# Kernel tuning notes

Measured on AMD Instinct MI355X. Metric: run time of the kernel, lower is better.

Reference implementation:

```python
import jax, jax.numpy as jnp
import numpy as np

N_NODES = 100000
N_EDGES = 1600000
N_GRAPHS = 512
F_IN = 20
HID = 128
OUT = HID // 2


def _glorot(key, shape):
    fan_in, fan_out = shape[0], shape[1]
    lim = float(np.sqrt(6.0 / (fan_in + fan_out)))
    return jax.random.uniform(key, shape, jnp.float32, -lim, lim)


def setup_inputs() -> dict:
    key = jax.random.key(0)
    ks = jax.random.split(key, 12)
    x = jax.random.normal(ks[0], (N_NODES, F_IN), jnp.float32)
    edge_index = jax.random.randint(ks[1], (2, N_EDGES), 0, N_NODES, dtype=jnp.int64)
    batch = jnp.sort(jax.random.randint(ks[2], (N_NODES,), 0, N_GRAPHS, dtype=jnp.int64))
    return {
        "x": x,
        "edge_index": edge_index,
        "batch": batch,
        "W1": _glorot(ks[3], (F_IN, HID)), "b1": jnp.zeros((HID,), jnp.float32),
        "W2": _glorot(ks[4], (HID, HID)), "b2": jnp.zeros((HID,), jnp.float32),
        "W3": _glorot(ks[5], (HID, HID)), "b3": jnp.zeros((HID,), jnp.float32),
        "Wout": _glorot(ks[6], (HID, OUT)), "bout": jnp.zeros((OUT,), jnp.float32),
    }


def _gcn_conv(x, W, b, src, dst, num_nodes):
    # PyG GCNConv: x' = D^{-1/2} (A + I) D^{-1/2} X W + b (self-loops already in src/dst)
    xw = x @ W                                                  # [N, H]
    ones = jnp.ones(src.shape[0], dtype=xw.dtype)
    deg = jax.ops.segment_sum(ones, dst, num_segments=num_nodes)
    dinv = jnp.where(deg > 0, jax.lax.rsqrt(deg), 0.0)          # [N]
    norm = dinv[src] * dinv[dst]                                # [E+N]
    msg = xw[src] * norm[:, None]                               # gather + scale
    return jax.ops.segment_sum(msg, dst, num_segments=num_nodes) + b


def reference(x, edge_index, batch, W1, b1, W2, b2, W3, b3, Wout, bout):
    num_nodes = x.shape[0]
    loops = jnp.arange(num_nodes, dtype=edge_index.dtype)
    src = jnp.concatenate([edge_index[0], loops])
    dst = jnp.concatenate([edge_index[1], loops])

    h = jax.nn.relu(_gcn_conv(x, W1, b1, src, dst, num_nodes))
    h = jax.nn.relu(_gcn_conv(h, W2, b2, src, dst, num_nodes))
    h = jax.nn.relu(_gcn_conv(h, W3, b3, src, dst, num_nodes))

    # global_mean_pool over graph ids
    sums = jax.ops.segment_sum(h, batch, num_segments=N_GRAPHS)
    counts = jax.ops.segment_sum(jnp.ones(num_nodes, h.dtype), batch, num_segments=N_GRAPHS)
    pooled = sums / jnp.maximum(counts, 1.0)[:, None]           # [G, H]
    return pooled @ Wout + bout                                 # [G, H//2]
```

## Files before the change

### kernel.cpp

```cpp
#include <hip/hip_runtime.h>
#include <hip/hip_fp16.h>

#define N_NODES 100000
#define N_EDGES 1600000
#define N_GRAPHS 512
#define F_IN 20
#define HID 128
#define OUT_F 64

#define BUCKETS 512
#define SPAN 196
#define BCAP 3500
#define EPB 4096

typedef _Float16 half8_t __attribute__((ext_vector_type(8)));
typedef float f32x4_t __attribute__((ext_vector_type(4)));
typedef unsigned int uv4 __attribute__((ext_vector_type(4)));

__device__ inline float4 h4_to_f4(uint2 u) {
    __half2 h0 = *(__half2*)&u.x;
    __half2 h1 = *(__half2*)&u.y;
    float2 f0 = __half22float2(h0);
    float2 f1 = __half22float2(h1);
    return make_float4(f0.x, f0.y, f1.x, f1.y);
}

__device__ inline float4 f4_from(unsigned a, unsigned b) {
    __half2 h0 = *(__half2*)&a;
    __half2 h1 = *(__half2*)&b;
    float2 f0 = __half22float2(h0);
    float2 f1 = __half22float2(h1);
    return make_float4(f0.x, f0.y, f1.x, f1.y);
}

__device__ inline void acc8(float4& aL, float4& aH, uv4 v) {
    float4 l_ = f4_from(v[0], v[1]);
    float4 h_ = f4_from(v[2], v[3]);
    aL.x += l_.x; aL.y += l_.y; aL.z += l_.z; aL.w += l_.w;
    aH.x += h_.x; aH.y += h_.y; aH.z += h_.z; aH.w += h_.w;
}

__global__ __launch_bounds__(512) void partition(const int* __restrict__ src,
                                                 const int* __restrict__ dst,
                                                 int* __restrict__ bpairs,
                                                 int* cur512) {
    __shared__ int lcnt[8][BUCKETS];
    __shared__ int woff[8][BUCKETS];
    int t = threadIdx.x;
    int wv = t >> 6;
    for (int i = t; i < 8 * BUCKETS; i += 512) ((int*)lcnt)[i] = 0;
    __syncthreads();
    int base = blockIdx.x * EPB;
    int myb[8], myp[8], myr[8];
#pragma unroll
    for (int i = 0; i < 8; ++i) {
        int e = base + i * 512 + t;
        int b = -1, p = 0, rk = 0;
        if (e < N_EDGES) {
            int s = src[e], d = dst[e];
            b = d / SPAN;
            p = (s << 9) | (d - b * SPAN);
            rk = atomicAdd(&lcnt[wv][b], 1);
        }
        myb[i] = b; myp[i] = p; myr[i] = rk;
    }
    __syncthreads();
    {
        int c[8], tot = 0;
#pragma unroll
        for (int w = 0; w < 8; ++w) { c[w] = lcnt[w][t]; tot += c[w]; }
        int gb = atomicAdd(&cur512[t], tot);
#pragma unroll
        for (int w = 0; w < 8; ++w) { woff[w][t] = gb; gb += c[w]; }
    }
    __syncthreads();
#pragma unroll
    for (int i = 0; i < 8; ++i) {
        int b = myb[i];
        if (b >= 0) {
            int p = woff[wv][b] + myr[i];
            if (p < BCAP) bpairs[(size_t)b * BCAP + p] = myp[i];
        }
    }
}

__global__ __launch_bounds__(512) void csr_build(const int* __restrict__ bpairs,
                                                 const int* __restrict__ cur512,
                                                 int* __restrict__ row_st,
                                                 int* __restrict__ csr,
                                                 const float* __restrict__ x,
                                                 __half* __restrict__ Xs) {
    __shared__ int ocnt[SPAN];
    __shared__ int sc[512];
    __shared__ int cur[SPAN];
    __shared__ int sbase;
    int b = blockIdx.x, t = threadIdx.x;

    int myc = cur512[t];
    sc[t] = myc;
    __syncthreads();
    for (int o = 1; o < BUCKETS; o <<= 1) {
        int v = (t >= o) ? sc[t - o] : 0;
        __syncthreads();
        sc[t] += v;
        __syncthreads();
    }
    if (t == b) sbase = sc[t] - myc;
    if (b == BUCKETS - 1 && t == 0) row_st[N_NODES] = N_EDGES;

    int n0 = b * SPAN;
    int span = N_NODES - n0; if (span > SPAN) span = SPAN;
    if (span < 0) span = 0;
    if (t < SPAN) ocnt[t] = 0;
    __syncthreads();

    int n = cur512[b];
    if (n > BCAP) n = BCAP;
    const int* p = bpairs + (size_t)b * BCAP;
    for (int i = t; i < n; i += 512) atomicAdd(&ocnt[p[i] & 511], 1);
    __syncthreads();
    sc[t] = (t < span) ? ocnt[t] : 0;
    __syncthreads();
    for (int o = 1; o < 512; o <<= 1) {
        int v = (t >= o) ? sc[t - o] : 0;
        __syncthreads();
        sc[t] += v;
        __syncthreads();
    }
    int base = sbase;
    if (t < span) {
        int start = sc[t] - ocnt[t];
        row_st[n0 + t] = base + start;
        cur[t] = start;
    }
    __syncthreads();
    for (int i = t; i < n; i += 512) {
        int e = p[i];
        int lp = atomicAdd(&cur[e & 511], 1);
        csr[base + lp] = e >> 9;
    }
    for (int i = t; i < span * 32; i += 512) {
        int nl = i >> 5, f = i & 31;
        float v = (f < F_IN) ? x[(size_t)(n0 + nl) * F_IN + f] : 0.f;
        float di = rsqrtf((float)(ocnt[nl] + 1));
        Xs[(size_t)(n0 + nl) * 32 + f] = __float2half(di * v);
    }
}

__global__ __launch_bounds__(256) void w_prep(const float* __restrict__ W2,
                                              const float* __restrict__ W3,
                                              _Float16* __restrict__ Whl) {
    int idx = blockIdx.x * 256 + threadIdx.x;
    if (idx >= 2 * HID * HID) return;
    int layer = idx >> 14;
    int c = (idx >> 7) & 127;
    int k = idx & 127;
    float w = (layer ? W3 : W2)[k * HID + c];
    _Float16 hi = (_Float16)w;
    _Float16 lo = (_Float16)((w - (float)hi) * 2048.0f);
    Whl[((size_t)layer * 2 + 0) * 16384 + c * 128 + k] = hi;
    Whl[((size_t)layer * 2 + 1) * 16384 + c * 128 + k] = lo;
}

__global__ __launch_bounds__(256) void layer1(const __half* __restrict__ Xs,
                                              const int* __restrict__ row_st,
                                              const int* __restrict__ csr,
                                              const float* __restrict__ W,
                                              const float* __restrict__ bias,
                                              __half* __restrict__ H) {
    __shared__ float Wlds[F_IN * HID];
    __shared__ float Alds[64][F_IN];
    __shared__ float d1[64];
    const int t = threadIdx.x;
    const int node0 = blockIdx.x * 64;

    for (int i = t; i < F_IN * HID; i += 256) Wlds[i] = W[i];

    const int grp = t >> 2;
    const int l   = t & 3;
    const int n   = node0 + grp;
    float di = 0.f;
    if (n < N_NODES) {
        int r0 = row_st[n], r1 = row_st[n + 1];
        const uv4* X4 = (const uv4*)Xs;
        uv4 u = X4[(size_t)n * 4 + l];
        float4 accL = f4_from(u[0], u[1]);
        float4 accH = f4_from(u[2], u[3]);
        int r = r0;
        for (; r + 7 < r1; r += 8) {
            int s0 = csr[r],     s1 = csr[r + 1], s2 = csr[r + 2], s3 = csr[r + 3];
            int s4 = csr[r + 4], s5 = csr[r + 5], s6 = csr[r + 6], s7 = csr[r + 7];
            uv4 vv0 = X4[(size_t)s0 * 4 + l];
            uv4 vv1 = X4[(size_t)s1 * 4 + l];
            uv4 vv2 = X4[(size_t)s2 * 4 + l];
            uv4 vv3 = X4[(size_t)s3 * 4 + l];
            uv4 vv4 = X4[(size_t)s4 * 4 + l];
            uv4 vv5 = X4[(size_t)s5 * 4 + l];
            uv4 vv6 = X4[(size_t)s6 * 4 + l];
            uv4 vv7 = X4[(size_t)s7 * 4 + l];
            uv4 vv[8] = {vv0, vv1, vv2, vv3, vv4, vv5, vv6, vv7};
#pragma unroll
            for (int j = 0; j < 8; ++j) acc8(accL, accH, vv[j]);
        }
        for (; r < r1; ++r) acc8(accL, accH, X4[(size_t)csr[r] * 4 + l]);
        di = rsqrtf((float)(r1 - r0 + 1));
        if (l < 2) {
            int f0 = l * 8;
            Alds[grp][f0 + 0] = di * accL.x;
            Alds[grp][f0 + 1] = di * accL.y;
            Alds[grp][f0 + 2] = di * accL.z;
            Alds[grp][f0 + 3] = di * accL.w;
            Alds[grp][f0 + 4] = di * accH.x;
            Alds[grp][f0 + 5] = di * accH.y;
            Alds[grp][f0 + 6] = di * accH.z;
            Alds[grp][f0 + 7] = di * accH.w;
        } else if (l == 2) {
            Alds[grp][16] = di * accL.x;
            Alds[grp][17] = di * accL.y;
            Alds[grp][18] = di * accL.z;
            Alds[grp][19] = di * accL.w;
        }
    }
    if (l == 0) d1[grp] = di;
    __syncthreads();

    const int nl = t >> 2;
    const int cb = (t & 3) * 4;
    float4 acc[8];
#pragma unroll
    for (int j = 0; j < 8; ++j) acc[j] = *(const float4*)&bias[cb + 16 * j];
#pragma unroll
    for (int k = 0; k < F_IN; ++k) {
        float a = Alds[nl][k];
        const float* Wr = &Wlds[k * HID + cb];
#pragma unroll
        for (int j = 0; j < 8; ++j) {
            float4 w = *(const float4*)&Wr[16 * j];
            acc[j].x = fmaf(a, w.x, acc[j].x);
            acc[j].y = fmaf(a, w.y, acc[j].y);
            acc[j].z = fmaf(a, w.z, acc[j].z);
            acc[j].w = fmaf(a, w.w, acc[j].w);
        }
    }
    if (node0 + nl < N_NODES) {
        float dd = d1[nl];
#pragma unroll
        for (int j = 0; j < 8; ++j) {
            float vx = fmaxf(acc[j].x, 0.f) * dd;
            float vy = fmaxf(acc[j].y, 0.f) * dd;
            float vz = fmaxf(acc[j].z, 0.f) * dd;
            float vw = fmaxf(acc[j].w, 0.f) * dd;
            __half2 h0 = __floats2half2_rn(vx, vy);
            __half2 h1 = __floats2half2_rn(vz, vw);
            uint2 u; u.x = *(unsigned*)&h0; u.y = *(unsigned*)&h1;
            ((uint2*)H)[(size_t)(node0 + nl) * 32 + (t & 3) + 4 * j] = u;
        }
    }
}

template<int APPLY_D>
__global__ __launch_bounds__(512) void layer_fused(const __half* __restrict__ P,
                                                   const int* __restrict__ row_st,
                                                   const int* __restrict__ csr,
                                                   const _Float16* __restrict__ Wb,
                                                   const float* __restrict__ bias,
                                                   __half* __restrict__ Pout) {
    __shared__ __align__(16) _Float16 Alds[64 * 128];
    __shared__ float dls[64];
    const int t = threadIdx.x;
    const int node0 = blockIdx.x * 64;

    {
        const int grp = t >> 3, l = t & 7;
        const int n = node0 + grp;
        float4 a0 = {0,0,0,0}, a1 = {0,0,0,0}, a2 = {0,0,0,0}, a3 = {0,0,0,0};
        float di = 0.f;
        if (n < N_NODES) {
            int r0 = row_st[n], r1 = row_st[n + 1];
            di = rsqrtf((float)(r1 - r0 + 1));
            const uv4* P4 = (const uv4*)P;
            uv4 u0 = P4[(size_t)n * 16 + l];
            uv4 u1 = P4[(size_t)n * 16 + 8 + l];
            a0 = f4_from(u0[0], u0[1]); a1 = f4_from(u0[2], u0[3]);
            a2 = f4_from(u1[0], u1[1]); a3 = f4_from(u1[2], u1[3]);
            int r = r0;
            for (; r + 3 < r1; r += 4) {
                int s0 = csr[r], s1 = csr[r + 1], s2 = csr[r + 2], s3 = csr[r + 3];
                uv4 p00 = P4[(size_t)s0 * 16 + l];
                uv4 p01 = P4[(size_t)s0 * 16 + 8 + l];
                uv4 p10 = P4[(size_t)s1 * 16 + l];
                uv4 p11 = P4[(size_t)s1 * 16 + 8 + l];
                uv4 p20 = P4[(size_t)s2 * 16 + l];
                uv4 p21 = P4[(size_t)s2 * 16 + 8 + l];
                uv4 p30 = P4[(size_t)s3 * 16 + l];
                uv4 p31 = P4[(size_t)s3 * 16 + 8 + l];
                acc8(a0, a1, p00); acc8(a2, a3, p01);
                acc8(a0, a1, p10); acc8(a2, a3, p11);
                acc8(a0, a1, p20); acc8(a2, a3, p21);
                acc8(a0, a1, p30); acc8(a2, a3, p31);
            }
            for (; r < r1; ++r) {
                int s = csr[r];
                acc8(a0, a1, P4[(size_t)s * 16 + l]);
                acc8(a2, a3, P4[(size_t)s * 16 + 8 + l]);
            }
        }
        a0.x *= di; a0.y *= di; a0.z *= di; a0.w *= di;
        a1.x *= di; a1.y *= di; a1.z *= di; a1.w *= di;
        a2.x *= di; a2.y *= di; a2.z *= di; a2.w *= di;
        a3.x *= di; a3.y *= di; a3.z *= di; a3.w *= di;
        __half2 h0 = __floats2half2_rn(a0.x, a0.y), h1 = __floats2half2_rn(a0.z, a0.w);
        __half2 h2 = __floats2half2_rn(a1.x, a1.y), h3 = __floats2half2_rn(a1.z, a1.w);
        __half2 h4 = __floats2half2_rn(a2.x, a2.y), h5 = __floats2half2_rn(a2.z, a2.w);
        __half2 h6 = __floats2half2_rn(a3.x, a3.y), h7 = __floats2half2_rn(a3.z, a3.w);
        uv4 c0, c1;
        c0[0] = *(unsigned*)&h0; c0[1] = *(unsigned*)&h1;
        c0[2] = *(unsigned*)&h2; c0[3] = *(unsigned*)&h3;
        c1[0] = *(unsigned*)&h4; c1[1] = *(unsigned*)&h5;
        c1[2] = *(unsigned*)&h6; c1[3] = *(unsigned*)&h7;
        int swz = (grp & 7) << 4;
        char* rowp = (char*)Alds + grp * 256;
        *(uv4*)(rowp + ((l * 16) ^ swz)) = c0;
        *(uv4*)(rowp + ((128 + l * 16) ^ swz)) = c1;
        if (l == 0) dls[grp] = di;
    }
    __syncthreads();

    const int wv = t >> 6;
    const int ln = t & 63;
    const int lr = ln & 15;
    const int lq = ln >> 4;

    half8_t bh[4], bl[4];
    {
        const _Float16* wp = Wb + (size_t)(wv * 16 + lr) * 128 + lq * 8;
#pragma unroll
        for (int kc = 0; kc < 4; ++kc) {
            bh[kc] = *(const half8_t*)(wp + kc * 32);
            bl[kc] = *(const half8_t*)(wp + 16384 + kc * 32);
        }
    }
    f32x4_t acch[4], accl[4];
#pragma unroll
    for (int s = 0; s < 4; ++s) { acch[s] = (f32x4_t){0,0,0,0}; accl[s] = (f32x4_t){0,0,0,0}; }

#pragma unroll
    for (int strip = 0; strip < 4; ++strip) {
        const char* rowp = (const char*)Alds + (strip * 16 + lr) * 256;
        const int sw = (lr & 7) << 4;
#pragma unroll
        for (int kc = 0; kc < 4; ++kc) {
            half8_t a = *(const half8_t*)(rowp + ((kc * 64 + lq * 16) ^ sw));
            acch[strip] = __builtin_amdgcn_mfma_f32_16x16x32_f16(a, bh[kc], acch[strip], 0, 0, 0);
            accl[strip] = __builtin_amdgcn_mfma_f32_16x16x32_f16(a, bl[kc], accl[strip], 0, 0, 0);
        }
    }

    const float bc = bias[wv * 16 + lr];
#pragma unroll
    for (int strip = 0; strip < 4; ++strip) {
#pragma unroll
        for (int j = 0; j < 4; ++j) {
            int rowl = strip * 16 + lq * 4 + j;
            int row = node0 + rowl;
            if (row < N_NODES) {
                float v = acch[strip][j] + accl[strip][j] * 4.8828125e-4f + bc;
                v = fmaxf(v, 0.f);
                if (APPLY_D) v *= dls[rowl];
                Pout[(size_t)row * 128 + wv * 16 + lr] = __float2half(v);
            }
        }
    }
}

__global__ __launch_bounds__(256) void pool_head(const __half* __restrict__ H,
                                                 const int* __restrict__ batch,
                                                 const float* __restrict__ Wout,
                                                 const float* __restrict__ bout,
                                                 float* __restrict__ out) {
    __shared__ float4 part[8][32];
    __shared__ float p[HID];
    __shared__ int bounds[2];
    int g = blockIdx.x;
    int t = threadIdx.x;
    if (t < 2) {
        int target = g + t;
        int lo = 0, hi = N_NODES;
        while (lo < hi) {
            int mid = (lo + hi) >> 1;
            if (batch[mid] < target) lo = mid + 1; else hi = mid;
        }
        bounds[t] = lo;
    }
    __syncthreads();
    int lo = bounds[0], hi = bounds[1];
    int grp = t >> 5, l = t & 31;
    const uint2* Hf = (const uint2*)H;
    float4 acc = make_float4(0.f, 0.f, 0.f, 0.f);
    for (int n = lo + grp; n < hi; n += 8) {
        float4 v = h4_to_f4(Hf[(size_t)n * 32 + l]);
        acc.x += fmaxf(v.x, 0.f);
        acc.y += fmaxf(v.y, 0.f);
        acc.z += fmaxf(v.z, 0.f);
        acc.w += fmaxf(v.w, 0.f);
    }
    part[grp][l] = acc;
    __syncthreads();
    if (t < 32) {
        float4 s = part[0][t];
#pragma unroll
        for (int j = 1; j < 8; ++j) {
            float4 v = part[j][t];
            s.x += v.x; s.y += v.y; s.z += v.z; s.w += v.w;
        }
        float inv = 1.0f / fmaxf((float)(hi - lo), 1.0f);
        p[t * 4 + 0] = s.x * inv;
        p[t * 4 + 1] = s.y * inv;
        p[t * 4 + 2] = s.z * inv;
        p[t * 4 + 3] = s.w * inv;
    }
    __syncthreads();
    if (t < OUT_F) {
        float acc2 = 0.f;
#pragma unroll 8
        for (int k = 0; k < HID; ++k)
            acc2 = fmaf(p[k], Wout[k * OUT_F + t], acc2);
        out[g * OUT_F + t] = acc2 + bout[t];
    }
}

extern "C" void kernel_launch(void* const* d_in, const int* in_sizes, int n_in,
                              void* d_out, int out_size, void* d_ws, size_t ws_size,
                              hipStream_t stream) {
    const float* x     = (const float*)d_in[0];
    const int*   ei    = (const int*)d_in[1];
    const int*   batch = (const int*)d_in[2];
    const float* W1    = (const float*)d_in[3];
    const float* b1    = (const float*)d_in[4];
    const float* W2    = (const float*)d_in[5];
    const float* b2    = (const float*)d_in[6];
    const float* W3    = (const float*)d_in[7];
    const float* b3    = (const float*)d_in[8];
    const float* Wout  = (const float*)d_in[9];
    const float* bout  = (const float*)d_in[10];
    float* out = (float*)d_out;

    const int* src = ei;
    const int* dst = ei + N_EDGES;

    float* A      = (float*)d_ws;
    float* Breg   = A + (size_t)N_NODES * HID;
    int*   row_st = (int*)(Breg + (size_t)N_NODES * HID);
    int*   cur512 = row_st + N_NODES + 1;
    int*   csr    = cur512 + BUCKETS;

    int*      bpairs = (int*)A;
    __half*   Xs     = (__half*)((char*)A + 7168000);
    __half*   T      = (__half*)A;
    __half*   H      = (__half*)Breg;
    _Float16* Whl    = (_Float16*)((char*)A + 26u * 1024 * 1024);

    hipMemsetAsync(cur512, 0, BUCKETS * sizeof(int), stream);
    partition<<<(N_EDGES + EPB - 1) / EPB, 512, 0, stream>>>(src, dst, bpairs, cur512);
    w_prep<<<128, 256, 0, stream>>>(W2, W3, Whl);
    csr_build<<<BUCKETS, 512, 0, stream>>>(bpairs, cur512, row_st, csr, x, Xs);

    layer1<<<(N_NODES + 63) / 64, 256, 0, stream>>>(Xs, row_st, csr, W1, b1, H);

    layer_fused<1><<<(N_NODES + 63) / 64, 512, 0, stream>>>(H, row_st, csr, Whl, b2, T);
    layer_fused<0><<<(N_NODES + 63) / 64, 512, 0, stream>>>(T, row_st, csr, Whl + 32768, b3, H);

    pool_head<<<N_GRAPHS, 256, 0, stream>>>(H, batch, Wout, bout, out);
}
```

Measured before the change: 353.0 us.

## Shrink fused GCN layer blocks to 16 nodes with 2 waves

The fused aggregate+GEMM layer kernel now processes 16 nodes per block with 128 threads instead of 64 nodes with 512 threads. Each wave holds the A fragment in registers and loops over 4 output column tiles, loading weight fragments per tile instead of keeping them resident. Bounds checks are dropped because N_NODES divides evenly by 16. The smaller blocks are meant to spread the irregular gather work more finely and cut the barrier wait caused by the slowest node in a block. In exchange each block reloads weights more often, and there are four times as many blocks.

```diff
diff --git a/kernel.cpp b/kernel.cpp
--- a/kernel.cpp
+++ b/kernel.cpp
@@ -259,51 +259,47 @@
 }
 
 template<int APPLY_D>
-__global__ __launch_bounds__(512) void layer_fused(const __half* __restrict__ P,
+__global__ __launch_bounds__(128) void layer_fused(const __half* __restrict__ P,
                                                    const int* __restrict__ row_st,
                                                    const int* __restrict__ csr,
                                                    const _Float16* __restrict__ Wb,
                                                    const float* __restrict__ bias,
                                                    __half* __restrict__ Pout) {
-    __shared__ __align__(16) _Float16 Alds[64 * 128];
-    __shared__ float dls[64];
+    __shared__ __align__(16) _Float16 Alds[16 * 128];
+    __shared__ float dls[16];
     const int t = threadIdx.x;
-    const int node0 = blockIdx.x * 64;
+    const int node0 = blockIdx.x * 16;
 
     {
         const int grp = t >> 3, l = t & 7;
         const int n = node0 + grp;
-        float4 a0 = {0,0,0,0}, a1 = {0,0,0,0}, a2 = {0,0,0,0}, a3 = {0,0,0,0};
-        float di = 0.f;
-        if (n < N_NODES) {
-            int r0 = row_st[n], r1 = row_st[n + 1];
-            di = rsqrtf((float)(r1 - r0 + 1));
-            const uv4* P4 = (const uv4*)P;
-            uv4 u0 = P4[(size_t)n * 16 + l];
-            uv4 u1 = P4[(size_t)n * 16 + 8 + l];
-            a0 = f4_from(u0[0], u0[1]); a1 = f4_from(u0[2], u0[3]);
-            a2 = f4_from(u1[0], u1[1]); a3 = f4_from(u1[2], u1[3]);
-            int r = r0;
-            for (; r + 3 < r1; r += 4) {
-                int s0 = csr[r], s1 = csr[r + 1], s2 = csr[r + 2], s3 = csr[r + 3];
-                uv4 p00 = P4[(size_t)s0 * 16 + l];
-                uv4 p01 = P4[(size_t)s0 * 16 + 8 + l];
-                uv4 p10 = P4[(size_t)s1 * 16 + l];
-                uv4 p11 = P4[(size_t)s1 * 16 + 8 + l];
-                uv4 p20 = P4[(size_t)s2 * 16 + l];
-                uv4 p21 = P4[(size_t)s2 * 16 + 8 + l];
-                uv4 p30 = P4[(size_t)s3 * 16 + l];
-                uv4 p31 = P4[(size_t)s3 * 16 + 8 + l];
-                acc8(a0, a1, p00); acc8(a2, a3, p01);
-                acc8(a0, a1, p10); acc8(a2, a3, p11);
-                acc8(a0, a1, p20); acc8(a2, a3, p21);
-                acc8(a0, a1, p30); acc8(a2, a3, p31);
-            }
-            for (; r < r1; ++r) {
-                int s = csr[r];
-                acc8(a0, a1, P4[(size_t)s * 16 + l]);
-                acc8(a2, a3, P4[(size_t)s * 16 + 8 + l]);
-            }
+        int r0 = row_st[n], r1 = row_st[n + 1];
+        float di = rsqrtf((float)(r1 - r0 + 1));
+        const uv4* P4 = (const uv4*)P;
+        uv4 u0 = P4[(size_t)n * 16 + l];
+        uv4 u1 = P4[(size_t)n * 16 + 8 + l];
+        float4 a0 = f4_from(u0[0], u0[1]), a1 = f4_from(u0[2], u0[3]);
+        float4 a2 = f4_from(u1[0], u1[1]), a3 = f4_from(u1[2], u1[3]);
+        int r = r0;
+        for (; r + 3 < r1; r += 4) {
+            int s0 = csr[r], s1 = csr[r + 1], s2 = csr[r + 2], s3 = csr[r + 3];
+            uv4 p00 = P4[(size_t)s0 * 16 + l];
+            uv4 p01 = P4[(size_t)s0 * 16 + 8 + l];
+            uv4 p10 = P4[(size_t)s1 * 16 + l];
+            uv4 p11 = P4[(size_t)s1 * 16 + 8 + l];
+            uv4 p20 = P4[(size_t)s2 * 16 + l];
+            uv4 p21 = P4[(size_t)s2 * 16 + 8 + l];
+            uv4 p30 = P4[(size_t)s3 * 16 + l];
+            uv4 p31 = P4[(size_t)s3 * 16 + 8 + l];
+            acc8(a0, a1, p00); acc8(a2, a3, p01);
+            acc8(a0, a1, p10); acc8(a2, a3, p11);
+            acc8(a0, a1, p20); acc8(a2, a3, p21);
+            acc8(a0, a1, p30); acc8(a2, a3, p31);
+        }
+        for (; r < r1; ++r) {
+            int s = csr[r];
+            acc8(a0, a1, P4[(size_t)s * 16 + l]);
+            acc8(a2, a3, P4[(size_t)s * 16 + 8 + l]);
         }
         a0.x *= di; a0.y *= di; a0.z *= di; a0.w *= di;
         a1.x *= di; a1.y *= di; a1.z *= di; a1.w *= di;
@@ -331,44 +327,35 @@
     const int lr = ln & 15;
     const int lq = ln >> 4;
 
-    half8_t bh[4], bl[4];
+    half8_t afr[4];
     {
-        const _Float16* wp = Wb + (size_t)(wv * 16 + lr) * 128 + lq * 8;
+        const char* rowp = (const char*)Alds + lr * 256;
+        const int sw = (lr & 7) << 4;
+#pragma unroll
+        for (int kc = 0; kc < 4; ++kc)
+            afr[kc] = *(const half8_t*)(rowp + ((kc * 64 + lq * 16) ^ sw));
+    }
+#pragma unroll
+    for (int i = 0; i < 4; ++i) {
+        const int c0 = (wv * 4 + i) * 16;
+        const _Float16* wp = Wb + (size_t)(c0 + lr) * 128 + lq * 8;
+        f32x4_t acch = (f32x4_t){0, 0, 0, 0};
+        f32x4_t accl = (f32x4_t){0, 0, 0, 0};
 #pragma unroll
         for (int kc = 0; kc < 4; ++kc) {
-            bh[kc] = *(const half8_t*)(wp + kc * 32);
-            bl[kc] = *(const half8_t*)(wp + 16384 + kc * 32);
-        }
-    }
-    f32x4_t acch[4], accl[4];
-#pragma unroll
-    for (int s = 0; s < 4; ++s) { acch[s] = (f32x4_t){0,0,0,0}; accl[s] = (f32x4_t){0,0,0,0}; }
-
-#pragma unroll
-    for (int strip = 0; strip < 4; ++strip) {
-        const char* rowp = (const char*)Alds + (strip * 16 + lr) * 256;
-        const int sw = (lr & 7) << 4;
-#pragma unroll
-        for (int kc = 0; kc < 4; ++kc) {
-            half8_t a = *(const half8_t*)(rowp + ((kc * 64 + lq * 16) ^ sw));
-            acch[strip] = __builtin_amdgcn_mfma_f32_16x16x32_f16(a, bh[kc], acch[strip], 0, 0, 0);
-            accl[strip] = __builtin_amdgcn_mfma_f32_16x16x32_f16(a, bl[kc], accl[strip], 0, 0, 0);
-        }
-    }
-
-    const float bc = bias[wv * 16 + lr];
-#pragma unroll
-    for (int strip = 0; strip < 4; ++strip) {
+            half8_t bh = *(const half8_t*)(wp + kc * 32);
+            half8_t bl = *(const half8_t*)(wp + 16384 + kc * 32);
+            acch = __builtin_amdgcn_mfma_f32_16x16x32_f16(afr[kc], bh, acch, 0, 0, 0);
+            accl = __builtin_amdgcn_mfma_f32_16x16x32_f16(afr[kc], bl, accl, 0, 0, 0);
+        }
+        const float bc = bias[c0 + lr];
 #pragma unroll
         for (int j = 0; j < 4; ++j) {
-            int rowl = strip * 16 + lq * 4 + j;
-            int row = node0 + rowl;
-            if (row < N_NODES) {
-                float v = acch[strip][j] + accl[strip][j] * 4.8828125e-4f + bc;
-                v = fmaxf(v, 0.f);
-                if (APPLY_D) v *= dls[rowl];
-                Pout[(size_t)row * 128 + wv * 16 + lr] = __float2half(v);
-            }
+            int rowl = lq * 4 + j;
+            float v = acch[j] + accl[j] * 4.8828125e-4f + bc;
+            v = fmaxf(v, 0.f);
+            if (APPLY_D) v *= dls[rowl];
+            Pout[(size_t)(node0 + rowl) * 128 + c0 + lr] = __float2half(v);
         }
     }
 }
@@ -467,8 +454,8 @@
 
     layer1<<<(N_NODES + 63) / 64, 256, 0, stream>>>(Xs, row_st, csr, W1, b1, H);
 
-    layer_fused<1><<<(N_NODES + 63) / 64, 512, 0, stream>>>(H, row_st, csr, Whl, b2, T);
-    layer_fused<0><<<(N_NODES + 63) / 64, 512, 0, stream>>>(T, row_st, csr, Whl + 32768, b3, H);
+    layer_fused<1><<<N_NODES / 16, 128, 0, stream>>>(H, row_st, csr, Whl, b2, T);
+    layer_fused<0><<<N_NODES / 16, 128, 0, stream>>>(T, row_st, csr, Whl + 32768, b3, H);
 
     pool_head<<<N_GRAPHS, 256, 0, stream>>>(H, batch, Wout, bout, out);
 }
```

Result: slower. 373.4 us (+5.8%).
